# Performance work log

Hardware: AMD Instinct MI355X
Metric: run time of the kernel (lower is better)

## Reference

```python
import jax, jax.numpy as jnp
import numpy as np

EPS = 1e-12  # F.normalize clamp_min


def setup_inputs() -> dict:
    key = jax.random.key(0)
    k1, k2, k3, k4 = jax.random.split(key, 4)
    emb_dim = 64
    user_feat = jax.random.normal(k1, (4096, emb_dim), dtype=jnp.float32)
    seq_feat = jax.random.normal(k2, (2048, 32, emb_dim), dtype=jnp.float32)
    # nn.Linear(emb_dim, emb_dim): weight [out, in], bias [out]
    bound = 1.0 / np.sqrt(emb_dim)
    W = jax.random.uniform(k3, (emb_dim, emb_dim), dtype=jnp.float32, minval=-bound, maxval=bound)
    b = jax.random.uniform(k4, (emb_dim,), dtype=jnp.float32, minval=-bound, maxval=bound)
    return {"user_feat": user_feat, "seq_feat": seq_feat, "W": W, "b": b}


def reference(user_feat, seq_feat, W, b):
    D = seq_feat.shape[-1]
    sf = seq_feat.reshape(-1, D)                       # [M, D]
    M = sf.shape[0]
    # attention scores + L1 row-normalization (F.normalize p=1, dim=1)
    att = jnp.einsum('nd,md->nm', user_feat, sf)       # [N, M]
    att = att / jnp.maximum(jnp.sum(jnp.abs(att), axis=1, keepdims=True), EPS)
    # mean_m Linear(att[n,m] * sf[m]) == (att @ sf)/M @ W^T + b  (affine distributivity)
    agg = jnp.einsum('nm,md->nd', att, sf) / M         # [N, D]
    message_mean = agg @ W.T + b                        # [N, D]
    return user_feat + message_mean
```

## Files before the change

### kernel.cpp

```cpp
#include <hip/hip_runtime.h>
#include <hip/hip_bf16.h>

typedef __attribute__((ext_vector_type(8))) short short8v;
typedef __attribute__((ext_vector_type(4))) float f32x4;

#define N_ROWS 4096
#define M_ROWS 65536
#define DIM 64

#define AS1C(p) ((const __attribute__((address_space(1))) void*)(p))
#define AS3(p)  ((__attribute__((address_space(3))) void*)(p))
#define SCHED0() __builtin_amdgcn_sched_barrier(0)

__device__ inline unsigned short f2bf(float f) {
  unsigned u = __float_as_uint(f);
  unsigned r = (u + 0x7FFFu + ((u >> 16) & 1u)) >> 16;
  return (unsigned short)r;
}
__device__ inline float bf2f(unsigned short s) {
  return __uint_as_float(((unsigned)s) << 16);
}

__global__ __launch_bounds__(256) void cvt_g_kernel(const float* __restrict__ sf,
                                                    unsigned short* __restrict__ sf16,
                                                    float* __restrict__ Gp) {
  __shared__ unsigned short tile[128 * DIM];
  const int tid = threadIdx.x;
  const size_t base = (size_t)blockIdx.x * 128 * DIM;

#pragma unroll
  for (int j = 0; j < 8; ++j) {
    const int e = tid * 4 + j * 1024;
    float4 v = *reinterpret_cast<const float4*>(sf + base + e);
    ushort4 o;
    o.x = f2bf(v.x); o.y = f2bf(v.y); o.z = f2bf(v.z); o.w = f2bf(v.w);
    *reinterpret_cast<ushort4*>(sf16 + base + e) = o;
    *reinterpret_cast<ushort4*>(&tile[e]) = o;
  }
  __syncthreads();

  const int d1 = (tid & 15) * 4;
  const int d2 = (tid >> 4) * 4;
  float acc[4][4];
#pragma unroll
  for (int i = 0; i < 4; ++i)
#pragma unroll
    for (int j = 0; j < 4; ++j) acc[i][j] = 0.f;

#pragma unroll 8
  for (int m = 0; m < 128; ++m) {
    ushort4 a4 = *reinterpret_cast<const ushort4*>(&tile[m * DIM + d1]);
    ushort4 b4 = *reinterpret_cast<const ushort4*>(&tile[m * DIM + d2]);
    float a[4] = {bf2f(a4.x), bf2f(a4.y), bf2f(a4.z), bf2f(a4.w)};
    float b[4] = {bf2f(b4.x), bf2f(b4.y), bf2f(b4.z), bf2f(b4.w)};
#pragma unroll
    for (int i = 0; i < 4; ++i)
#pragma unroll
      for (int j = 0; j < 4; ++j) acc[i][j] += a[i] * b[j];
  }
#pragma unroll
  for (int i = 0; i < 4; ++i)
#pragma unroll
    for (int j = 0; j < 4; ++j)
      Gp[(size_t)blockIdx.x * 4096 + (d1 + i) * DIM + (d2 + j)] = acc[i][j];
}

__global__ __launch_bounds__(256, 4) void s_kernel(const float* __restrict__ u,
                                                   const unsigned short* __restrict__ sf16,
                                                   float* __restrict__ Spart) {
  __shared__ unsigned short Bt[4][4096];
  const int bn = blockIdx.x;
  const int bm = blockIdx.y;
  const int tid = threadIdx.x;
  const int wid = tid >> 6;
  const int lane = tid & 63;
  const int l15 = lane & 15;
  const int lg  = lane >> 4;
  const int n0 = bn * 256 + wid * 64;
  const int mbase = bm * 1024;

  short8v au[4][2];
#pragma unroll
  for (int st = 0; st < 4; ++st) {
#pragma unroll
    for (int kf = 0; kf < 2; ++kf) {
      const float* ap = u + (size_t)(n0 + st * 16 + l15) * DIM + kf * 32 + lg * 8;
      float4 f0 = *reinterpret_cast<const float4*>(ap);
      float4 f1 = *reinterpret_cast<const float4*>(ap + 4);
      short8v v;
      v[0] = (short)f2bf(f0.x); v[1] = (short)f2bf(f0.y);
      v[2] = (short)f2bf(f0.z); v[3] = (short)f2bf(f0.w);
      v[4] = (short)f2bf(f1.x); v[5] = (short)f2bf(f1.y);
      v[6] = (short)f2bf(f1.z); v[7] = (short)f2bf(f1.w);
      au[st][kf] = v;
    }
  }

  float sacc[4][4];
#pragma unroll
  for (int st = 0; st < 4; ++st)
#pragma unroll
    for (int r = 0; r < 4; ++r) sacc[st][r] = 0.f;
  const f32x4 ZERO = (f32x4){0.f, 0.f, 0.f, 0.f};

  const int kp0 = wid * 2, kp1 = wid * 2 + 1;
  const unsigned short* gp0 = sf16 + (size_t)(mbase + lane) * DIM + kp0 * 8;
  const unsigned short* gp1 = sf16 + (size_t)(mbase + lane) * DIM + kp1 * 8;

#define STAGE2(BUF)                                                            \
  {                                                                            \
    __builtin_amdgcn_global_load_lds(AS1C(gp0), AS3(&Bt[BUF][kp0 * 512]), 16, 0, 0); \
    __builtin_amdgcn_global_load_lds(AS1C(gp1), AS3(&Bt[BUF][kp1 * 512]), 16, 0, 0); \
    gp0 += 4096; gp1 += 4096;                                                  \
  }

#define ABSADD(S, A)                                                           \
  { float _a = (A); asm("v_add_f32_e64 %0, %0, |%1|" : "+v"(S) : "v"(_a)); }

  const int bofs = lg * 512 + l15 * 8;

#define STEP(BUF, LAST, STAGECODE)                                             \
  {                                                                            \
    if (LAST) { asm volatile("s_waitcnt vmcnt(0)" ::: "memory"); }             \
    else      { asm volatile("s_waitcnt vmcnt(2)" ::: "memory"); }             \
    __builtin_amdgcn_s_barrier();                                              \
    SCHED0();                                                                  \
    STAGECODE;                                                                 \
    {                                                                          \
      const unsigned short* B = &Bt[BUF][0];                                   \
      __builtin_amdgcn_s_setprio(1);                                           \
      _Pragma("unroll") for (int g = 0; g < 4; ++g) {                          \
        short8v b0 = *reinterpret_cast<const short8v*>(&B[bofs + g * 128]);    \
        short8v b1 = *reinterpret_cast<const short8v*>(&B[bofs + 2048 + g * 128]); \
        _Pragma("unroll") for (int st = 0; st < 4; ++st) {                     \
          f32x4 acc = __builtin_amdgcn_mfma_f32_16x16x32_bf16(au[st][0], b0, ZERO, 0, 0, 0); \
          acc = __builtin_amdgcn_mfma_f32_16x16x32_bf16(au[st][1], b1, acc, 0, 0, 0); \
          ABSADD(sacc[st][0], acc[0]);                                         \
          ABSADD(sacc[st][1], acc[1]);                                         \
          ABSADD(sacc[st][2], acc[2]);                                         \
          ABSADD(sacc[st][3], acc[3]);                                         \
        }                                                                      \
      }                                                                        \
      __builtin_amdgcn_s_setprio(0);                                           \
    }                                                                          \
  }

  STAGE2(0);
  STAGE2(1);

#pragma unroll 1
  for (int s4 = 0; s4 < 3; ++s4) {
    STEP(0, false, STAGE2(2));
    STEP(1, false, STAGE2(3));
    STEP(2, false, STAGE2(0));
    STEP(3, false, STAGE2(1));
  }
  STEP(0, false, STAGE2(2));
  STEP(1, false, STAGE2(3));
  STEP(2, false, (void)0);
  STEP(3, true,  (void)0);

#undef STEP
#undef STAGE2

#pragma unroll
  for (int off = 1; off < 16; off <<= 1) {
#pragma unroll
    for (int st = 0; st < 4; ++st) {
#pragma unroll
      for (int r = 0; r < 4; ++r)
        sacc[st][r] += __shfl_xor(sacc[st][r], off, 64);
    }
  }
  if (l15 == 0) {
#pragma unroll
    for (int st = 0; st < 4; ++st)
#pragma unroll
      for (int r = 0; r < 4; ++r)
        Spart[(size_t)(n0 + st * 16 + lg * 4 + r) * 64 + bm] = sacc[st][r];
  }
}

__global__ __launch_bounds__(256) void gp_reduce_p(const float* __restrict__ Gp,
                                                   const float* __restrict__ W,
                                                   float* __restrict__ P) {
  const int j = blockIdx.x;
  const int d = threadIdx.x & 63;
  const int q = threadIdx.x >> 6;
  float g = 0.f;
#pragma unroll 8
  for (int i = 0; i < 128; ++i)
    g += Gp[(size_t)(q + 4 * i) * 4096 + j * DIM + d];
  __shared__ float part[4][DIM];
  part[q][d] = g;
  __syncthreads();
  if (q == 0) {
    float row = part[0][d] + part[1][d] + part[2][d] + part[3][d];
    part[0][d] = row;
  }
  __syncthreads();
  if (q == 0) {
    float acc = 0.f;
#pragma unroll
    for (int k = 0; k < DIM; ++k) acc += part[0][k] * W[d * DIM + k];
    P[j * DIM + d] = acc;
  }
}

__global__ __launch_bounds__(256) void out_kernel(const float* __restrict__ u,
                                                  const float* __restrict__ P,
                                                  const float* __restrict__ Spart,
                                                  const float* __restrict__ bias,
                                                  float* __restrict__ out) {
  __shared__ float Ps[DIM][DIM];
  __shared__ float us[4][DIM];
  const int tid = threadIdx.x;
#pragma unroll
  for (int i = 0; i < 16; ++i)
    (&Ps[0][0])[tid + i * 256] = P[tid + i * 256];
  const int base = blockIdx.x * 256;
  us[tid >> 6][tid & 63] = u[base + tid];
  __syncthreads();

  const int nl = tid >> 6;
  const int d = tid & 63;
  const int n = blockIdx.x * 4 + nl;

  float sp = Spart[(size_t)n * 64 + d];
#pragma unroll
  for (int off = 1; off < 64; off <<= 1) sp += __shfl_xor(sp, off, 64);
  const float inv = 1.f / (fmaxf(sp, 1e-12f) * (float)M_ROWS);

  float acc = 0.f;
#pragma unroll
  for (int jj = 0; jj < DIM; ++jj) acc += us[nl][jj] * Ps[jj][d];
  out[base + tid] = us[nl][d] + acc * inv + bias[d];
}

extern "C" void kernel_launch(void* const* d_in, const int* in_sizes, int n_in,
                              void* d_out, int out_size, void* d_ws, size_t ws_size,
                              hipStream_t stream) {
  const float* u  = (const float*)d_in[0];
  const float* sf = (const float*)d_in[1];
  const float* W  = (const float*)d_in[2];
  const float* b  = (const float*)d_in[3];
  float* out = (float*)d_out;

  char* ws = (char*)d_ws;
  unsigned short* sf16 = (unsigned short*)ws;
  float* Spart = (float*)(ws + 8388608);
  float* Gp    = (float*)(ws + 9437184);
  float* P     = (float*)(ws + 17825792);

  cvt_g_kernel<<<dim3(512), 256, 0, stream>>>(sf, sf16, Gp);
  s_kernel<<<dim3(16, 64), 256, 0, stream>>>(u, sf16, Spart);
  gp_reduce_p<<<dim3(64), 256, 0, stream>>>(Gp, W, P);
  out_kernel<<<dim3(N_ROWS * 64 / 256), 256, 0, stream>>>(u, P, Spart, b, out);
}
```

Before: 125.4 us.

## Switch score kernel to 32x32x16 MFMA with triple-buffered LDS and new tiling

The L1-norm score kernel now uses 32x32x16 bf16 MFMAs, with each wave covering 32 user rows instead of 64. Each block handles 128 users and 2048 sequence rows on a 32x32 grid, and the LDS ring drops from four buffers to three. Each B fragment loaded from LDS now feeds a larger MFMA, which is meant to raise MFMA efficiency and cut LDS reads per flop. The trade-off is that A is reused less per wave, and the wider 16-register accumulators put more pressure on the abs-add reduction. Spart and out_kernel now reduce over 32 partials instead of 64.

Result: slower. 133.4 us (+6.3%).

```diff
diff --git a/kernel.cpp b/kernel.cpp
--- a/kernel.cpp
+++ b/kernel.cpp
@@ -3,6 +3,7 @@
 
 typedef __attribute__((ext_vector_type(8))) short short8v;
 typedef __attribute__((ext_vector_type(4))) float f32x4;
+typedef __attribute__((ext_vector_type(16))) float f32x16;
 
 #define N_ROWS 4096
 #define M_ROWS 65536
@@ -68,40 +69,37 @@
 __global__ __launch_bounds__(256, 4) void s_kernel(const float* __restrict__ u,
                                                    const unsigned short* __restrict__ sf16,
                                                    float* __restrict__ Spart) {
-  __shared__ unsigned short Bt[4][4096];
+  __shared__ unsigned short Bt[3][4096];
   const int bn = blockIdx.x;
   const int bm = blockIdx.y;
   const int tid = threadIdx.x;
   const int wid = tid >> 6;
   const int lane = tid & 63;
-  const int l15 = lane & 15;
-  const int lg  = lane >> 4;
-  const int n0 = bn * 256 + wid * 64;
-  const int mbase = bm * 1024;
-
-  short8v au[4][2];
-#pragma unroll
-  for (int st = 0; st < 4; ++st) {
-#pragma unroll
-    for (int kf = 0; kf < 2; ++kf) {
-      const float* ap = u + (size_t)(n0 + st * 16 + l15) * DIM + kf * 32 + lg * 8;
-      float4 f0 = *reinterpret_cast<const float4*>(ap);
-      float4 f1 = *reinterpret_cast<const float4*>(ap + 4);
-      short8v v;
-      v[0] = (short)f2bf(f0.x); v[1] = (short)f2bf(f0.y);
-      v[2] = (short)f2bf(f0.z); v[3] = (short)f2bf(f0.w);
-      v[4] = (short)f2bf(f1.x); v[5] = (short)f2bf(f1.y);
-      v[6] = (short)f2bf(f1.z); v[7] = (short)f2bf(f1.w);
-      au[st][kf] = v;
-    }
-  }
-
-  float sacc[4][4];
-#pragma unroll
-  for (int st = 0; st < 4; ++st)
-#pragma unroll
-    for (int r = 0; r < 4; ++r) sacc[st][r] = 0.f;
-  const f32x4 ZERO = (f32x4){0.f, 0.f, 0.f, 0.f};
+  const int lo = lane & 31;
+  const int hi = lane >> 5;
+  const int n0w = bn * 128 + wid * 32;
+  const int mbase = bm * 2048;
+
+  short8v au[4];
+#pragma unroll
+  for (int kk = 0; kk < 4; ++kk) {
+    const float* ap = u + (size_t)(n0w + lo) * DIM + kk * 16 + hi * 8;
+    float4 f0 = *reinterpret_cast<const float4*>(ap);
+    float4 f1 = *reinterpret_cast<const float4*>(ap + 4);
+    short8v v;
+    v[0] = (short)f2bf(f0.x); v[1] = (short)f2bf(f0.y);
+    v[2] = (short)f2bf(f0.z); v[3] = (short)f2bf(f0.w);
+    v[4] = (short)f2bf(f1.x); v[5] = (short)f2bf(f1.y);
+    v[6] = (short)f2bf(f1.z); v[7] = (short)f2bf(f1.w);
+    au[kk] = v;
+  }
+
+  float sacc[2][16];
+#pragma unroll
+  for (int mt = 0; mt < 2; ++mt)
+#pragma unroll
+    for (int r = 0; r < 16; ++r) sacc[mt][r] = 0.f;
+  const f32x16 ZERO16 = (f32x16)(0.f);
 
   const int kp0 = wid * 2, kp1 = wid * 2 + 1;
   const unsigned short* gp0 = sf16 + (size_t)(mbase + lane) * DIM + kp0 * 8;
@@ -116,8 +114,6 @@
 
 #define ABSADD(S, A)                                                           \
   { float _a = (A); asm("v_add_f32_e64 %0, %0, |%1|" : "+v"(S) : "v"(_a)); }
-
-  const int bofs = lg * 512 + l15 * 8;
 
 #define STEP(BUF, LAST, STAGECODE)                                             \
   {                                                                            \
@@ -129,17 +125,14 @@
     {                                                                          \
       const unsigned short* B = &Bt[BUF][0];                                   \
       __builtin_amdgcn_s_setprio(1);                                           \
-      _Pragma("unroll") for (int g = 0; g < 4; ++g) {                          \
-        short8v b0 = *reinterpret_cast<const short8v*>(&B[bofs + g * 128]);    \
-        short8v b1 = *reinterpret_cast<const short8v*>(&B[bofs + 2048 + g * 128]); \
-        _Pragma("unroll") for (int st = 0; st < 4; ++st) {                     \
-          f32x4 acc = __builtin_amdgcn_mfma_f32_16x16x32_bf16(au[st][0], b0, ZERO, 0, 0, 0); \
-          acc = __builtin_amdgcn_mfma_f32_16x16x32_bf16(au[st][1], b1, acc, 0, 0, 0); \
-          ABSADD(sacc[st][0], acc[0]);                                         \
-          ABSADD(sacc[st][1], acc[1]);                                         \
-          ABSADD(sacc[st][2], acc[2]);                                         \
-          ABSADD(sacc[st][3], acc[3]);                                         \
+      _Pragma("unroll") for (int mt = 0; mt < 2; ++mt) {                       \
+        f32x16 acc = ZERO16;                                                   \
+        _Pragma("unroll") for (int kk = 0; kk < 4; ++kk) {                     \
+          short8v b = *reinterpret_cast<const short8v*>(                       \
+              &B[(kk * 2 + hi) * 512 + (mt * 32 + lo) * 8]);                   \
+          acc = __builtin_amdgcn_mfma_f32_32x32x16_bf16(au[kk], b, acc, 0, 0, 0); \
         }                                                                      \
+        _Pragma("unroll") for (int r = 0; r < 16; ++r) ABSADD(sacc[mt][r], acc[r]); \
       }                                                                        \
       __builtin_amdgcn_s_setprio(0);                                           \
     }                                                                          \
@@ -149,35 +142,31 @@
   STAGE2(1);
 
 #pragma unroll 1
-  for (int s4 = 0; s4 < 3; ++s4) {
+  for (int s3 = 0; s3 < 10; ++s3) {
     STEP(0, false, STAGE2(2));
-    STEP(1, false, STAGE2(3));
-    STEP(2, false, STAGE2(0));
-    STEP(3, false, STAGE2(1));
-  }
-  STEP(0, false, STAGE2(2));
-  STEP(1, false, STAGE2(3));
-  STEP(2, false, (void)0);
-  STEP(3, true,  (void)0);
+    STEP(1, false, STAGE2(0));
+    STEP(2, false, STAGE2(1));
+  }
+  STEP(0, false, (void)0);
+  STEP(1, true,  (void)0);
 
 #undef STEP
 #undef STAGE2
 
 #pragma unroll
-  for (int off = 1; off < 16; off <<= 1) {
-#pragma unroll
-    for (int st = 0; st < 4; ++st) {
-#pragma unroll
-      for (int r = 0; r < 4; ++r)
-        sacc[st][r] += __shfl_xor(sacc[st][r], off, 64);
+  for (int r = 0; r < 16; ++r) sacc[0][r] += sacc[1][r];
+#pragma unroll
+  for (int off = 1; off < 32; off <<= 1) {
+#pragma unroll
+    for (int r = 0; r < 16; ++r)
+      sacc[0][r] += __shfl_xor(sacc[0][r], off, 64);
+  }
+  if (lo == 0) {
+#pragma unroll
+    for (int r = 0; r < 16; ++r) {
+      const int row = (r & 3) + 8 * (r >> 2) + 4 * hi;
+      Spart[(size_t)(n0w + row) * 32 + bm] = sacc[0][r];
     }
-  }
-  if (l15 == 0) {
-#pragma unroll
-    for (int st = 0; st < 4; ++st)
-#pragma unroll
-      for (int r = 0; r < 4; ++r)
-        Spart[(size_t)(n0 + st * 16 + lg * 4 + r) * 64 + bm] = sacc[st][r];
   }
 }
 
@@ -226,9 +215,9 @@
   const int d = tid & 63;
   const int n = blockIdx.x * 4 + nl;
 
-  float sp = Spart[(size_t)n * 64 + d];
-#pragma unroll
-  for (int off = 1; off < 64; off <<= 1) sp += __shfl_xor(sp, off, 64);
+  float sp = Spart[(size_t)n * 32 + (d & 31)];
+#pragma unroll
+  for (int off = 1; off < 32; off <<= 1) sp += __shfl_xor(sp, off, 64);
   const float inv = 1.f / (fmaxf(sp, 1e-12f) * (float)M_ROWS);
 
   float acc = 0.f;
@@ -253,7 +242,7 @@
   float* P     = (float*)(ws + 17825792);
 
   cvt_g_kernel<<<dim3(512), 256, 0, stream>>>(sf, sf16, Gp);
-  s_kernel<<<dim3(16, 64), 256, 0, stream>>>(u, sf16, Spart);
+  s_kernel<<<dim3(32, 32), 256, 0, stream>>>(u, sf16, Spart);
   gp_reduce_p<<<dim3(64), 256, 0, stream>>>(Gp, W, P);
   out_kernel<<<dim3(N_ROWS * 64 / 256), 256, 0, stream>>>(u, P, Spart, b, out);
 }
```
